# Kernel tuning notes

Hardware: AMD Instinct MI355X
Metric: run time of the kernel (lower is better)

Reference implementation:

```python
import jax, jax.numpy as jnp
import numpy as np

DIM = 192          # out_dim
HEADS = 8          # num_heads (split into 2 branches of 4)
SS = (4, 8)        # split_size
B, HH, WW, CIN = 8, 128, 128, 192


def calc_mask(H, W, wh, ww):
    # Swin-style shift mask for windows of (wh, ww), shift (wh//2, ww//2).
    sh, sw = wh // 2, ww // 2
    h = jnp.arange(H)
    w = jnp.arange(W)
    hreg = (h >= H - wh).astype(jnp.int32) + (h >= H - sh).astype(jnp.int32)
    wreg = (w >= W - ww).astype(jnp.int32) + (w >= W - sw).astype(jnp.int32)
    img = hreg[:, None] * 3 + wreg[None, :]                      # (H, W) region ids
    win = img.reshape(H // wh, wh, W // ww, ww).transpose(0, 2, 1, 3).reshape(-1, wh * ww)
    return jnp.where(win[:, :, None] != win[:, None, :], -100.0, 0.0)  # (nW, N, N)


def window_attention(q, k, v, mask, d, Hsp, Wsp):
    # q,k,v: (B, C, H, W); mask: (u*v, N, N); d heads, window Hsp x Wsp
    Bc, C, H, W = k.shape
    u, vv = H // Hsp, W // Wsp
    c = C // d
    N = Hsp * Wsp
    scale = c ** -0.5

    def v2w(t):  # 'b (d c) (u h) (v w) -> (b u v) d (h w) c'
        return t.reshape(Bc, d, c, u, Hsp, vv, Wsp).transpose(0, 3, 5, 1, 4, 6, 2).reshape(Bc * u * vv, d, N, c)

    qw, kw, vw = v2w(q), v2w(k), v2w(v)
    attn = jnp.einsum('ndic,ndjc->ndij', qw, kw) * scale          # (B*u*v, d, N, N)
    attn = attn.reshape(Bc, u * vv, d, N, N) + mask[None, :, None, :, :]
    a = jax.nn.softmax(attn, axis=-1).reshape(Bc * u * vv, d, N, N)
    o = jnp.einsum('ndij,ndjc->ndic', a, vw)
    # '(b u v) d (h w) c -> b (d c) (u h) (v w)'
    return o.reshape(Bc, u, vv, d, Hsp, Wsp, c).transpose(0, 3, 6, 1, 4, 2, 5).reshape(Bc, C, H, W)


def setup_inputs() -> dict:
    key = jax.random.key(0)
    k0, k1, k2, k3 = jax.random.split(key, 4)
    x = jax.random.normal(k0, (B, HH * WW, CIN), dtype=jnp.float32)
    Wq = jax.random.normal(k1, (CIN, DIM), dtype=jnp.float32) * 0.02
    Wkv = jax.random.normal(k2, (CIN, 2 * DIM), dtype=jnp.float32) * 0.02
    Wproj = jax.random.normal(k3, (DIM, DIM), dtype=jnp.float32) * 0.02
    bproj = jnp.zeros((DIM,), dtype=jnp.float32)
    return {"x": x, "Wq": Wq, "Wkv": Wkv, "Wproj": Wproj, "bproj": bproj, "H": HH, "W": WW}


def reference(x, Wq, Wkv, Wproj, bproj, H, W):
    Bc, L, _ = x.shape
    C = Wq.shape[1]
    q = (x @ Wq).reshape(Bc, H, W, C).transpose(0, 3, 1, 2)       # (B, C, H, W)
    kv = (x @ Wkv).reshape(Bc, H, W, 2, C)
    k = kv[..., 0, :].transpose(0, 3, 1, 2)
    v = kv[..., 1, :].transpose(0, 3, 1, 2)

    Ch = C // 2
    s0, s1 = SS[0] // 2, SS[1] // 2
    roll0 = lambda t: jnp.roll(t, (-s0, -s1), axis=(-2, -1))
    roll1 = lambda t: jnp.roll(t, (-s1, -s0), axis=(-2, -1))
    mask0 = calc_mask(H, W, SS[0], SS[1])   # branch 0: 4x8 windows
    mask1 = calc_mask(H, W, SS[1], SS[0])   # branch 1: 8x4 windows
    d = HEADS // 2

    x0 = window_attention(roll0(q[:, :Ch]), roll0(k[:, :Ch]), roll0(v[:, :Ch]), mask0, d, SS[0], SS[1])
    x1 = window_attention(roll1(q[:, Ch:]), roll1(k[:, Ch:]), roll1(v[:, Ch:]), mask1, d, SS[1], SS[0])
    x0 = jnp.roll(x0, (s0, s1), axis=(-2, -1))
    x1 = jnp.roll(x1, (s1, s0), axis=(-2, -1))

    out = jnp.concatenate([x0, x1], axis=1)                        # (B, C, H, W)
    out = out.transpose(0, 2, 3, 1).reshape(Bc, L, C)
    return out @ Wproj + bproj
```

## Files before the change

### kernel.cpp

```cpp
#include <hip/hip_runtime.h>
#include <hip/hip_bf16.h>
#include <stdint.h>

typedef __bf16 bf16;
typedef __bf16 bf16x8 __attribute__((ext_vector_type(8)));
typedef __bf16 bf16x4 __attribute__((ext_vector_type(4)));
typedef float  f32x4  __attribute__((ext_vector_type(4)));

#define MROWS 131072

__device__ __forceinline__ f32x4 mfma16(bf16x8 a, bf16x8 b, f32x4 c) {
    return __builtin_amdgcn_mfma_f32_16x16x32_bf16(a, b, c, 0, 0, 0);
}
__device__ __forceinline__ f32x4 zero4() {
    f32x4 z; z[0]=0.f; z[1]=0.f; z[2]=0.f; z[3]=0.f; return z;
}
__device__ __forceinline__ bf16x8 zero8() {
    bf16x8 z;
#pragma unroll
    for (int i = 0; i < 8; ++i) z[i] = (bf16)0.f;
    return z;
}
template <int CTRL>
__device__ __forceinline__ float rowror(float x) {
    return __int_as_float(
        __builtin_amdgcn_mov_dpp(__float_as_int(x), CTRL, 0xF, 0xF, false));
}
__device__ __forceinline__ float rowsum16(float s) {
    s += rowror<0x128>(s);
    s += rowror<0x124>(s);
    s += rowror<0x122>(s);
    s += rowror<0x121>(s);
    return s;
}

__global__ void kw_transpose(const float* __restrict__ Wq, const float* __restrict__ Wkv,
                             const float* __restrict__ Wp, bf16* __restrict__ Wt,
                             bf16* __restrict__ Wpt) {
    int col = blockIdx.x;
    int k = threadIdx.x;
    if (col < 192)      Wt[col * 192 + k] = (bf16)Wq[k * 192 + col];
    else if (col < 576) Wt[col * 192 + k] = (bf16)Wkv[k * 384 + (col - 192)];
    else                Wpt[(col - 576) * 192 + k] = (bf16)Wp[k * 192 + (col - 576)];
}

__global__ __launch_bounds__(256, 4) void kfused(const float* __restrict__ X,
                                                 const bf16* __restrict__ Wt,
                                                 bf16* __restrict__ Out) {
    const int bid = blockIdx.x;
    const int slab = bid & 7;
    const int t = bid >> 3;
    const int img = t >> 7;
    const int idx = t & 127;
    int branch, wa, wb;
    if (idx < 64) {
        branch = 0; wa = slab * 4 + (idx >> 4); wb = idx & 15;
    } else {
        branch = 1; int j = idx - 64; wa = slab * 2 + (j >> 5); wb = j & 31;
    }
    const int wh = branch ? 8 : 4, ww = branch ? 4 : 8;
    const int lww = branch ? 2 : 3;
    const int sh = wh >> 1, sw = ww >> 1;

    __shared__ __align__(16) char smem[20480];
    bf16 (*xs)[200]    = (bf16(*)[200])smem;
    bf16 (*qs)[104]    = (bf16(*)[104])smem;
    bf16 (*kss)[104]   = (bf16(*)[104])(smem + 6656);
    bf16 (*pl)[32][40] = (bf16(*)[32][40])smem;
    bf16 (*vt)[36]     = (bf16(*)[36])(smem + 13312);
    bf16 (*ob)[104]    = (bf16(*)[104])(smem + 13312);
    int* pix = (int*)(smem + 20224);
    int* rid = (int*)(smem + 20352);

    const int tid = threadIdx.x;
    const int hd = tid >> 6;
    const int l = tid & 63, li = l & 15, lk = l >> 4;

    if (tid < 32) {
        int ih = tid >> lww, iw = tid & (ww - 1);
        int hh = wa * wh + ih, wp = wb * ww + iw;
        int hreg = (hh >= 128 - wh) + (hh >= 128 - sh);
        int wreg = (wp >= 128 - ww) + (wp >= 128 - sw);
        rid[tid] = hreg * 3 + wreg;
        int srh = (hh + sh) & 127, srw = (wp + sw) & 127;
        pix[tid] = img * 16384 + srh * 128 + srw;
    }

#pragma unroll
    for (int i = 0; i < 3; ++i) {
        int c = tid + i * 256;
        int row = c / 24, col8 = (c % 24) * 8;
        int ih = row >> lww, iw = row & (ww - 1);
        int hh = wa * wh + ih, wp = wb * ww + iw;
        int srh = (hh + sh) & 127, srw = (wp + sw) & 127;
        const float* p = X + (size_t)(img * 16384 + srh * 128 + srw) * 192 + col8;
        f32x4 f0 = *(const f32x4*)p;
        f32x4 f1 = *(const f32x4*)(p + 4);
        bf16x8 v;
#pragma unroll
        for (int e = 0; e < 4; ++e) { v[e] = (bf16)f0[e]; v[4 + e] = (bf16)f1[e]; }
        *(bf16x8*)&xs[row][col8] = v;
    }
    __syncthreads();

    bf16x8 xf[2][6];
#pragma unroll
    for (int mt = 0; mt < 2; ++mt)
#pragma unroll
        for (int ks = 0; ks < 6; ++ks)
            xf[mt][ks] = *(const bf16x8*)&xs[mt * 16 + li][ks * 32 + lk * 8];

#define LOADW(dst, nt) {                                                            \
        int seg_ = (nt) / 6, cwi_ = ((nt) % 6) * 16;                                \
        const bf16* wr = Wt + (size_t)(seg_ * 192 + branch * 96 + cwi_ + li) * 192  \
                            + lk * 8;                                               \
        _Pragma("unroll")                                                           \
        for (int ks = 0; ks < 6; ++ks) dst[ks] = *(const bf16x8*)(wr + ks * 32);    \
    }
#define MFMA_SCATTER(frag, nt) {                                                    \
        f32x4 a0 = zero4(), a1 = zero4();                                           \
        _Pragma("unroll")                                                           \
        for (int ks = 0; ks < 6; ++ks) {                                            \
            a0 = mfma16(frag[ks], xf[0][ks], a0);                                   \
            a1 = mfma16(frag[ks], xf[1][ks], a1);                                   \
        }                                                                           \
        int seg_ = (nt) / 6, cwi_ = ((nt) % 6) * 16;                                \
        if (seg_ < 2) {                                                             \
            bf16 (*dst)[104] = (seg_ == 0) ? qs : kss;                              \
            bf16x4 p0, p1;                                                          \
            _Pragma("unroll")                                                       \
            for (int r = 0; r < 4; ++r) { p0[r] = (bf16)a0[r]; p1[r] = (bf16)a1[r]; } \
            *(bf16x4*)&dst[li][cwi_ + lk * 4] = p0;                                 \
            *(bf16x4*)&dst[16 + li][cwi_ + lk * 4] = p1;                            \
        } else {                                                                    \
            _Pragma("unroll")                                                       \
            for (int r = 0; r < 4; ++r) {                                           \
                int vc = cwi_ + lk * 4 + r;                                         \
                vt[vc][li] = (bf16)a0[r];                                           \
                vt[vc][16 + li] = (bf16)a1[r];                                      \
            }                                                                       \
        }                                                                           \
    }

    bf16x8 cur[6], nxt[6];
    LOADW(cur, hd);
    __syncthreads();

#pragma unroll
    for (int j = 0; j < 4; ++j) {
        int nt = hd + 4 * j;
        if (j < 3) {
            LOADW(nxt, nt + 4);
        } else if (hd < 2) {
            LOADW(nxt, nt + 4);
        }
        MFMA_SCATTER(cur, nt);
#pragma unroll
        for (int ks = 0; ks < 6; ++ks) cur[ks] = nxt[ks];
    }
    if (hd < 2) {
        MFMA_SCATTER(cur, hd + 16);
    }
    __syncthreads();

    bf16x8 aq[2], bk[2];
#pragma unroll
    for (int t2 = 0; t2 < 2; ++t2) {
        if (lk < 3) {
            aq[t2] = *(const bf16x8*)&qs[t2 * 16 + li][hd * 24 + lk * 8];
            bk[t2] = *(const bf16x8*)&kss[t2 * 16 + li][hd * 24 + lk * 8];
        } else {
            aq[t2] = zero8();
            bk[t2] = zero8();
        }
    }
    f32x4 s[2][2];
#pragma unroll
    for (int it = 0; it < 2; ++it)
#pragma unroll
        for (int jt = 0; jt < 2; ++jt) s[it][jt] = mfma16(aq[it], bk[jt], zero4());

    __syncthreads();

    const float scale = 0.2041241452319315f;
    const int r0 = lk * 4;
    const int rj0 = rid[li], rj1 = rid[16 + li];
    float inv_[2][4];
#pragma unroll
    for (int it = 0; it < 2; ++it) {
#pragma unroll
        for (int r = 0; r < 4; ++r) {
            int i = it * 16 + r0 + r;
            int ri = rid[i];
            float v0 = s[it][0][r] * scale + ((ri != rj0) ? -100.f : 0.f);
            float v1 = s[it][1][r] * scale + ((ri != rj1) ? -100.f : 0.f);
            float e0 = __expf(v0), e1 = __expf(v1);
            pl[hd][i][li] = (bf16)e0;
            pl[hd][i][16 + li] = (bf16)e1;
            float sm = rowsum16(e0 + e1);
            inv_[it][r] = 1.f / sm;
        }
    }

    bf16x8 ap[2], bv[2];
#pragma unroll
    for (int it = 0; it < 2; ++it)
        ap[it] = *(const bf16x8*)&pl[hd][it * 16 + li][lk * 8];
#pragma unroll
    for (int ct = 0; ct < 2; ++ct) {
        int col = ct * 16 + li;
        if (col > 23) col = 23;
        bv[ct] = *(const bf16x8*)&vt[hd * 24 + col][lk * 8];
    }
    f32x4 o[2][2];
#pragma unroll
    for (int it = 0; it < 2; ++it)
#pragma unroll
        for (int ct = 0; ct < 2; ++ct) o[it][ct] = mfma16(ap[it], bv[ct], zero4());

    __syncthreads();

#pragma unroll
    for (int it = 0; it < 2; ++it)
#pragma unroll
        for (int ct = 0; ct < 2; ++ct) {
            int col = ct * 16 + li;
            if (col < 24) {
#pragma unroll
                for (int r = 0; r < 4; ++r)
                    ob[it * 16 + r0 + r][hd * 24 + col] =
                        (bf16)(o[it][ct][r] * inv_[it][r]);
            }
        }
    __syncthreads();
    for (int c = tid; c < 384; c += 256) {
        int row = c / 12, ch = c % 12;
        *(bf16x8*)(Out + (size_t)pix[row] * 192 + branch * 96 + ch * 8) =
            *(const bf16x8*)&ob[row][ch * 8];
    }
#undef LOADW
#undef MFMA_SCATTER
}

#define BSTR 200
__global__ __launch_bounds__(256, 4) void kproj(const bf16* __restrict__ Ab,
                                                const bf16* __restrict__ Wpt,
                                                const float* __restrict__ bias,
                                                float* __restrict__ Out) {
    __shared__ __align__(16) bf16 Bs[96][BSTR];
    const int lid = blockIdx.x;
    const int xcd = lid & 7, s = lid >> 3;
    const int mg = xcd * 128 + s / 2;
    const int nb = s & 1;
    const int tid = threadIdx.x;
    const int w = tid >> 6, l = tid & 63, li = l & 15, lk = l >> 4;
    const int rb = mg * 128 + w * 32;
    const int cb = nb * 96;

    bf16x8 a[2][6];
#pragma unroll
    for (int it = 0; it < 2; ++it)
#pragma unroll
        for (int ks = 0; ks < 6; ++ks)
            a[it][ks] = *(const bf16x8*)(Ab + (size_t)(rb + it * 16 + li) * 192 + ks * 32 + lk * 8);

#pragma unroll
    for (int i = 0; i < 9; ++i) {
        int c = i * 256 + tid;
        int r = c / 24, col = (c % 24) * 8;
        *(bf16x8*)&Bs[r][col] = *(const bf16x8*)(Wpt + (size_t)(cb + r) * 192 + col);
    }
    __syncthreads();

    f32x4 acc[2][6];
#pragma unroll
    for (int it = 0; it < 2; ++it)
#pragma unroll
        for (int nt = 0; nt < 6; ++nt) acc[it][nt] = zero4();

#pragma unroll
    for (int nt = 0; nt < 6; ++nt) {
#pragma unroll
        for (int ks = 0; ks < 6; ++ks) {
            bf16x8 b = *(const bf16x8*)&Bs[nt * 16 + li][ks * 32 + lk * 8];
            acc[0][nt] = mfma16(b, a[0][ks], acc[0][nt]);
            acc[1][nt] = mfma16(b, a[1][ks], acc[1][nt]);
        }
    }

#pragma unroll
    for (int nt = 0; nt < 6; ++nt) {
        f32x4 bv4 = *(const f32x4*)(bias + cb + nt * 16 + lk * 4);
#pragma unroll
        for (int it = 0; it < 2; ++it) {
            f32x4 ov = acc[it][nt];
#pragma unroll
            for (int r = 0; r < 4; ++r) ov[r] += bv4[r];
            *(f32x4*)(Out + (size_t)(rb + it * 16 + li) * 192 + cb + nt * 16 + lk * 4) = ov;
        }
    }
}

extern "C" void kernel_launch(void* const* d_in, const int* in_sizes, int n_in,
                              void* d_out, int out_size, void* d_ws, size_t ws_size,
                              hipStream_t stream) {
    const float* x    = (const float*)d_in[0];
    const float* Wq   = (const float*)d_in[1];
    const float* Wkv  = (const float*)d_in[2];
    const float* Wp   = (const float*)d_in[3];
    const float* bias = (const float*)d_in[4];
    float* out = (float*)d_out;

    bf16* Ab  = (bf16*)d_ws;
    bf16* Wt  = Ab + (size_t)MROWS * 192;
    bf16* Wpt = Wt + 576 * 192;

    hipLaunchKernelGGL(kw_transpose, dim3(768), dim3(192), 0, stream, Wq, Wkv, Wp, Wt, Wpt);
    hipLaunchKernelGGL(kfused, dim3(8192), dim3(256), 0, stream, x, Wt, Ab);
    hipLaunchKernelGGL(kproj, dim3(2048), dim3(256), 0, stream, Ab, Wpt, bias, out);
}
```

Baseline: 145.9 us.

## Split QKV projection work across waves by row half and add MFMA priority hints

```diff
diff --git a/kernel.cpp b/kernel.cpp
--- a/kernel.cpp
+++ b/kernel.cpp
@@ -103,12 +103,12 @@
     }
     __syncthreads();
 
-    bf16x8 xf[2][6];
-#pragma unroll
-    for (int mt = 0; mt < 2; ++mt)
-#pragma unroll
-        for (int ks = 0; ks < 6; ++ks)
-            xf[mt][ks] = *(const bf16x8*)&xs[mt * 16 + li][ks * 32 + lk * 8];
+    const int mhalf = hd & 1;
+    const int tbase = hd >> 1;
+    bf16x8 xf[6];
+#pragma unroll
+    for (int ks = 0; ks < 6; ++ks)
+        xf[ks] = *(const bf16x8*)&xs[mhalf * 16 + li][ks * 32 + lk * 8];
 
 #define LOADW(dst, nt) {                                                            \
         int seg_ = (nt) / 6, cwi_ = ((nt) % 6) * 16;                                \
@@ -117,49 +117,34 @@
         _Pragma("unroll")                                                           \
         for (int ks = 0; ks < 6; ++ks) dst[ks] = *(const bf16x8*)(wr + ks * 32);    \
     }
-#define MFMA_SCATTER(frag, nt) {                                                    \
-        f32x4 a0 = zero4(), a1 = zero4();                                           \
-        _Pragma("unroll")                                                           \
-        for (int ks = 0; ks < 6; ++ks) {                                            \
-            a0 = mfma16(frag[ks], xf[0][ks], a0);                                   \
-            a1 = mfma16(frag[ks], xf[1][ks], a1);                                   \
-        }                                                                           \
-        int seg_ = (nt) / 6, cwi_ = ((nt) % 6) * 16;                                \
-        if (seg_ < 2) {                                                             \
-            bf16 (*dst)[104] = (seg_ == 0) ? qs : kss;                              \
-            bf16x4 p0, p1;                                                          \
-            _Pragma("unroll")                                                       \
-            for (int r = 0; r < 4; ++r) { p0[r] = (bf16)a0[r]; p1[r] = (bf16)a1[r]; } \
-            *(bf16x4*)&dst[li][cwi_ + lk * 4] = p0;                                 \
-            *(bf16x4*)&dst[16 + li][cwi_ + lk * 4] = p1;                            \
-        } else {                                                                    \
-            _Pragma("unroll")                                                       \
-            for (int r = 0; r < 4; ++r) {                                           \
-                int vc = cwi_ + lk * 4 + r;                                         \
-                vt[vc][li] = (bf16)a0[r];                                           \
-                vt[vc][16 + li] = (bf16)a1[r];                                      \
-            }                                                                       \
-        }                                                                           \
-    }
 
     bf16x8 cur[6], nxt[6];
-    LOADW(cur, hd);
-    __syncthreads();
-
-#pragma unroll
-    for (int j = 0; j < 4; ++j) {
-        int nt = hd + 4 * j;
-        if (j < 3) {
-            LOADW(nxt, nt + 4);
-        } else if (hd < 2) {
-            LOADW(nxt, nt + 4);
-        }
-        MFMA_SCATTER(cur, nt);
+    LOADW(cur, tbase);
+    __syncthreads();
+
+#pragma unroll
+    for (int j = 0; j < 9; ++j) {
+        int nt = tbase + 2 * j;
+        if (j < 8) LOADW(nxt, nt + 2);
+        __builtin_amdgcn_s_setprio(1);
+        f32x4 a0 = zero4();
+#pragma unroll
+        for (int ks = 0; ks < 6; ++ks) a0 = mfma16(cur[ks], xf[ks], a0);
+        __builtin_amdgcn_s_setprio(0);
+        int seg_ = nt / 6, cwi_ = (nt % 6) * 16;
+        if (seg_ < 2) {
+            bf16 (*dst)[104] = (seg_ == 0) ? qs : kss;
+            bf16x4 p0;
+#pragma unroll
+            for (int r = 0; r < 4; ++r) p0[r] = (bf16)a0[r];
+            *(bf16x4*)&dst[mhalf * 16 + li][cwi_ + lk * 4] = p0;
+        } else {
+#pragma unroll
+            for (int r = 0; r < 4; ++r)
+                vt[cwi_ + lk * 4 + r][mhalf * 16 + li] = (bf16)a0[r];
+        }
 #pragma unroll
         for (int ks = 0; ks < 6; ++ks) cur[ks] = nxt[ks];
-    }
-    if (hd < 2) {
-        MFMA_SCATTER(cur, hd + 16);
     }
     __syncthreads();
 
@@ -174,11 +159,13 @@
             bk[t2] = zero8();
         }
     }
+    __builtin_amdgcn_s_setprio(1);
     f32x4 s[2][2];
 #pragma unroll
     for (int it = 0; it < 2; ++it)
 #pragma unroll
         for (int jt = 0; jt < 2; ++jt) s[it][jt] = mfma16(aq[it], bk[jt], zero4());
+    __builtin_amdgcn_s_setprio(0);
 
     __syncthreads();
 
@@ -212,11 +199,13 @@
         if (col > 23) col = 23;
         bv[ct] = *(const bf16x8*)&vt[hd * 24 + col][lk * 8];
     }
+    __builtin_amdgcn_s_setprio(1);
     f32x4 o[2][2];
 #pragma unroll
     for (int it = 0; it < 2; ++it)
 #pragma unroll
         for (int ct = 0; ct < 2; ++ct) o[it][ct] = mfma16(ap[it], bv[ct], zero4());
+    __builtin_amdgcn_s_setprio(0);
 
     __syncthreads();
 
@@ -239,7 +228,6 @@
             *(const bf16x8*)&ob[row][ch * 8];
     }
 #undef LOADW
-#undef MFMA_SCATTER
 }
 
 #define BSTR 200
```

Measured after the change: 237.6 us. 62.9% more time.
